# Performance work log

Measured on AMD Instinct MI355X. Metric: run time of the kernel, lower is better.

The kernel has to match this reference:

```python
import jax, jax.numpy as jnp
import numpy as np

N_OUT = 100000 - 1  # 99999, as hard-coded in the torch module
LEAK = 0.01         # torch LeakyReLU default slope


def setup_inputs() -> dict:
    key = jax.random.key(0)
    k1, k2, k3, k4, k5 = jax.random.split(key, 5)
    B, D = 512, 512
    H = D // 2
    x = jax.random.normal(k1, (B, D), dtype=jnp.float32)
    # torch.nn.Linear-style init scale ~ 1/sqrt(fan_in)
    w2 = jax.random.normal(k2, (H, D), dtype=jnp.float32) / np.sqrt(D)
    b2 = jax.random.normal(k3, (H,), dtype=jnp.float32) / np.sqrt(D)
    w3 = jax.random.normal(k4, (55, H), dtype=jnp.float32) / np.sqrt(H)
    b3 = jax.random.normal(k5, (55,), dtype=jnp.float32) / np.sqrt(H)
    return {"x": x, "w2": w2, "b2": b2, "w3": w3, "b3": b3}


def _digit_tables():
    # Static integer tables for i in [0, N_OUT).
    i = np.arange(N_OUT, dtype=np.int32)
    ndig = ((i >= 10).astype(np.int32) + (i >= 100) + (i >= 1000) + (i >= 10000)).astype(np.int32)
    ndig[0] = 1  # special case in the original code: i==0 -> n=1
    return jnp.asarray(i), jnp.asarray(ndig)


def reference(x, w2, b2, w3, b3):
    # tiny MLP (batched; equivalent to the per-sample torch loop)
    h = x @ w2.T + b2
    h = jnp.where(h >= 0, h, LEAK * h)          # LeakyReLU
    z = h @ w3.T + b3                            # [B, 55]
    p_len = jax.nn.softmax(z[:, :5], axis=-1)    # length distribution (5)
    p_dig = jax.nn.softmax(z[:, 5:].reshape(-1, 5, 10), axis=-1)  # 5 digit groups of 10
    x3 = jnp.concatenate([p_len, p_dig.reshape(-1, 50)], axis=-1)  # [B, 55]

    i, ndig = _digit_tables()                    # [N], [N]
    out = jnp.take(x3, ndig, axis=1)             # lead factor x3[k, n_i] -> [B, N]
    # Multiply the first n_i digit probabilities (original drops the last digit).
    for j in range(4):                           # max usable digits: n<=4
        expo = jnp.maximum(ndig - j, 0)
        d = (i // jnp.power(10, expo)) % 10      # j-th most significant digit
        idx = 5 + d + 10 * j                     # index into x3 digit groups
        factor = jnp.take(x3, idx, axis=1)       # [B, N]
        valid = (j < ndig)[None, :]
        out = out * jnp.where(valid, factor, 1.0)
    return out
```

## Files before the change

### kernel.cpp

```cpp
#include <hip/hip_runtime.h>
#include <hip/hip_bf16.h>


#define BATCH 512
#define DIM   512
#define HID   256
#define NCLS  55
#define NOUT  99999
#define LEAK  0.01f

__global__ __launch_bounds__(256) void mlp_x3_kernel(
    const float* __restrict__ x,  const float* __restrict__ w2,
    const float* __restrict__ b2, const float* __restrict__ w3,
    const float* __restrict__ b3, float* __restrict__ x3out) {
    __shared__ float xs[DIM];
    __shared__ float hs[HID];
    __shared__ float zp[4][NCLS];
    __shared__ float x3s[NCLS];

    const int tid = threadIdx.x;
    const int k   = blockIdx.x;

    xs[tid]       = x[(size_t)k * DIM + tid];
    xs[tid + 256] = x[(size_t)k * DIM + tid + 256];
    __syncthreads();

    {
        const float4* w2r = (const float4*)(w2 + (size_t)tid * DIM);
        const float4* xr  = (const float4*)xs;
        float4 a4 = make_float4(0.f, 0.f, 0.f, 0.f);
#pragma unroll 8
        for (int d4 = 0; d4 < DIM / 4; ++d4) {
            float4 w  = w2r[d4];
            float4 xv = xr[d4];
            a4.x += w.x * xv.x; a4.y += w.y * xv.y;
            a4.z += w.z * xv.z; a4.w += w.w * xv.w;
        }
        float acc = (a4.x + a4.y) + (a4.z + a4.w) + b2[tid];
        hs[tid] = (acc >= 0.f) ? acc : LEAK * acc;
    }
    __syncthreads();

    if (tid < 4 * NCLS) {
        int o = tid % NCLS, part = tid / NCLS;
        const float4* w3r = (const float4*)(w3 + (size_t)o * HID + part * 64);
        const float4* hr  = (const float4*)(hs + part * 64);
        float4 a4 = make_float4(0.f, 0.f, 0.f, 0.f);
#pragma unroll
        for (int d4 = 0; d4 < 16; ++d4) {
            float4 w = w3r[d4];
            float4 h = hr[d4];
            a4.x += w.x * h.x; a4.y += w.y * h.y;
            a4.z += w.z * h.z; a4.w += w.w * h.w;
        }
        zp[part][o] = (a4.x + a4.y) + (a4.z + a4.w);
    }
    __syncthreads();
    if (tid < NCLS)
        x3s[tid] = zp[0][tid] + zp[1][tid] + zp[2][tid] + zp[3][tid] + b3[tid];
    __syncthreads();

    if (tid < 6) {
        int off = (tid == 0) ? 0 : 5 + 10 * (tid - 1);
        int len = (tid == 0) ? 5 : 10;
        float m = -1e30f;
        for (int u = 0; u < len; ++u) m = fmaxf(m, x3s[off + u]);
        float s = 0.f;
        for (int u = 0; u < len; ++u) {
            float e = __expf(x3s[off + u] - m);
            x3s[off + u] = e;
            s += e;
        }
        float inv = 1.f / s;
        for (int u = 0; u < len; ++u) x3s[off + u] *= inv;
    }
    __syncthreads();

    if (tid < NCLS) x3out[k * NCLS + tid] = x3s[tid];
}

__device__ __forceinline__ float Vj(
    unsigned j, const float* __restrict__ T4A, const float* __restrict__ T3A,
    const float* __restrict__ T2A, const float* __restrict__ B4,
    const float* __restrict__ B3,  const float* __restrict__ A1b) {
    if (j >= 1000u) { unsigned q = j / 100u; return T4A[q] * B4[j - q * 100u]; }
    if (j >= 100u)  { unsigned q = j / 10u;  return T3A[q] * B3[j - q * 10u]; }
    if (j >= 10u)   return T2A[j];
    return A1b[j];
}

__global__ __launch_bounds__(256) void expand_kernel(
    const float* __restrict__ x3g, float* __restrict__ out) {
    __shared__ float T4A[100], T3A[100], T2A[100], B4[100];
    __shared__ float B3[16], A1b[16];
    __shared__ float x3s[NCLS];

    const int tid = threadIdx.x;
    const int k   = blockIdx.x >> 3;
    const int s   = blockIdx.x & 7;

    if (tid < NCLS) x3s[tid] = x3g[k * NCLS + tid];
    __syncthreads();

    if (tid < 100) {
        int hi = tid / 10, lo = tid % 10;
        float pp = x3s[5 + hi] * x3s[15 + lo];
        T4A[tid] = x3s[4] * pp;
        T3A[tid] = x3s[3] * pp;
        T2A[tid] = x3s[2] * pp;
        B4[tid]  = x3s[25 + hi] * x3s[35 + lo];
    } else if (tid < 110) {
        int d = tid - 100;
        B3[d]  = x3s[25 + d];
        A1b[d] = (d == 0) ? x3s[0] : x3s[1] * x3s[5 + d];
    }
    __syncthreads();

    const float pz = x3s[1] * x3s[5];

    const unsigned e_lo = (unsigned)s * 12500u;
    const unsigned n_el = (s == 7) ? 12499u : 12500u;
    const size_t   gbase = (size_t)k * NOUT + e_lo;
    const unsigned head = (unsigned)((4u - ((unsigned)gbase & 3u)) & 3u);
    const unsigned ng   = (n_el - head) >> 2;
    const unsigned tail0 = head + (ng << 2);

    if (tid < (int)head) {
        unsigned i = e_lo + (unsigned)tid;
        float v = Vj(i / 10u, T4A, T3A, T2A, B4, B3, A1b);
        if (i == 0u) v = pz;
        out[gbase + tid] = v;
    }
    if (tid < (int)(n_el - tail0)) {
        unsigned e = tail0 + (unsigned)tid;
        unsigned i = e_lo + e;
        out[gbase + e] = Vj(i / 10u, T4A, T3A, T2A, B4, B3, A1b);
    }

    float4* outv = (float4*)(out + gbase + head);
    for (unsigned g = tid; g < ng; g += 256) {
        unsigned i   = e_lo + head + (g << 2);
        unsigned j0  = i / 10u;
        unsigned rem = i - j0 * 10u;
        float v0 = Vj(j0, T4A, T3A, T2A, B4, B3, A1b);
        unsigned j1 = j0 + (rem >= 7u ? 1u : 0u);
        float v1 = Vj(j1, T4A, T3A, T2A, B4, B3, A1b);
        unsigned m = 10u - rem;
        float4 v;
        v.x = (i == 0u) ? pz : v0;
        v.y = (1u < m) ? v0 : v1;
        v.z = (2u < m) ? v0 : v1;
        v.w = (3u < m) ? v0 : v1;
        outv[g] = v;
    }
}

extern "C" void kernel_launch(void* const* d_in, const int* in_sizes, int n_in,
                              void* d_out, int out_size, void* d_ws, size_t ws_size,
                              hipStream_t stream) {
    const float* x  = (const float*)d_in[0];
    const float* w2 = (const float*)d_in[1];
    const float* b2 = (const float*)d_in[2];
    const float* w3 = (const float*)d_in[3];
    const float* b3 = (const float*)d_in[4];
    float* out = (float*)d_out;
    float* x3  = (float*)d_ws;

    mlp_x3_kernel<<<BATCH, 256, 0, stream>>>(x, w2, b2, w3, b3, x3);
    expand_kernel<<<BATCH * 8, 256, 0, stream>>>(x3, out);
}
```

Before: 244.6 us.

## Use wave-cooperative coalesced dot products with shuffle reductions in MLP kernel

Rewrites both MLP layers so each wavefront reads a weight row with all 64 lanes (coalesced float4 loads) and reduces with xor-shuffles, instead of one thread per output row striding through memory. This targets uncoalesced per-thread row reads of w2 and w3. The cost is 6 shuffle steps per output row and a serial loop over 64 rows per wave, which adds latency to a small kernel. The expand kernel, likely the dominant cost given the large output write, is unchanged.

```diff
diff --git a/kernel.cpp b/kernel.cpp
--- a/kernel.cpp
+++ b/kernel.cpp
@@ -15,49 +15,50 @@
     const float* __restrict__ b3, float* __restrict__ x3out) {
     __shared__ float xs[DIM];
     __shared__ float hs[HID];
-    __shared__ float zp[4][NCLS];
     __shared__ float x3s[NCLS];
 
-    const int tid = threadIdx.x;
-    const int k   = blockIdx.x;
+    const int tid  = threadIdx.x;
+    const int k    = blockIdx.x;
+    const int wave = tid >> 6;
+    const int lane = tid & 63;
 
     xs[tid]       = x[(size_t)k * DIM + tid];
     xs[tid + 256] = x[(size_t)k * DIM + tid + 256];
     __syncthreads();
 
     {
-        const float4* w2r = (const float4*)(w2 + (size_t)tid * DIM);
-        const float4* xr  = (const float4*)xs;
-        float4 a4 = make_float4(0.f, 0.f, 0.f, 0.f);
-#pragma unroll 8
-        for (int d4 = 0; d4 < DIM / 4; ++d4) {
-            float4 w  = w2r[d4];
-            float4 xv = xr[d4];
-            a4.x += w.x * xv.x; a4.y += w.y * xv.y;
-            a4.z += w.z * xv.z; a4.w += w.w * xv.w;
+        float4 xv0 = ((const float4*)xs)[lane];
+        float4 xv1 = ((const float4*)xs)[lane + 64];
+        float  biasv = b2[wave * 64 + lane];
+        float  acc = 0.f;
+#pragma unroll 4
+        for (int t = 0; t < 64; ++t) {
+            const int n = wave * 64 + t;
+            const float4* w2r = (const float4*)(w2 + (size_t)n * DIM);
+            float4 a = w2r[lane];
+            float4 b = w2r[lane + 64];
+            float s = a.x * xv0.x + a.y * xv0.y + a.z * xv0.z + a.w * xv0.w
+                    + b.x * xv1.x + b.y * xv1.y + b.z * xv1.z + b.w * xv1.w;
+#pragma unroll
+            for (int off = 1; off < 64; off <<= 1) s += __shfl_xor(s, off, 64);
+            if (lane == t) acc = s;
         }
-        float acc = (a4.x + a4.y) + (a4.z + a4.w) + b2[tid];
-        hs[tid] = (acc >= 0.f) ? acc : LEAK * acc;
+        float hv = acc + biasv;
+        hs[wave * 64 + lane] = (hv >= 0.f) ? hv : LEAK * hv;
     }
     __syncthreads();
 
-    if (tid < 4 * NCLS) {
-        int o = tid % NCLS, part = tid / NCLS;
-        const float4* w3r = (const float4*)(w3 + (size_t)o * HID + part * 64);
-        const float4* hr  = (const float4*)(hs + part * 64);
-        float4 a4 = make_float4(0.f, 0.f, 0.f, 0.f);
+    {
+        float4 hv = ((const float4*)hs)[lane];
+        for (int o = wave; o < NCLS; o += 4) {
+            const float4* w3r = (const float4*)(w3 + (size_t)o * HID);
+            float4 w = w3r[lane];
+            float s = w.x * hv.x + w.y * hv.y + w.z * hv.z + w.w * hv.w;
 #pragma unroll
-        for (int d4 = 0; d4 < 16; ++d4) {
-            float4 w = w3r[d4];
-            float4 h = hr[d4];
-            a4.x += w.x * h.x; a4.y += w.y * h.y;
-            a4.z += w.z * h.z; a4.w += w.w * h.w;
+            for (int off = 1; off < 64; off <<= 1) s += __shfl_xor(s, off, 64);
+            if (lane == 0) x3s[o] = s + b3[o];
         }
-        zp[part][o] = (a4.x + a4.y) + (a4.z + a4.w);
     }
-    __syncthreads();
-    if (tid < NCLS)
-        x3s[tid] = zp[0][tid] + zp[1][tid] + zp[2][tid] + zp[3][tid] + b3[tid];
     __syncthreads();
 
     if (tid < 6) {
```

After: 236.2 us. 1.04x faster.
